# Kernel tuning notes

Hardware: AMD Instinct MI355X
Metric: run time of the kernel (lower is better)

## Reference

```python
import jax, jax.numpy as jnp
import numpy as np

N_NODES = 100000
N_EDGES = 1600000
IN_DIM = 128
HIDDEN = 128
EPS = 1e-5  # BatchNorm1d default eps


def gcn_conv(x, src, dst, W, b, n_nodes):
    """PyG GCNConv with default add_self_loops=True, edge_weight=None.
    out = D^{-1/2} (A + I) D^{-1/2} X W + b, deg computed from dst (col)."""
    xw = x @ W  # [N, out_dim] -- transform before propagate, as in PyG
    ones = jnp.ones((src.shape[0],), dtype=x.dtype)
    deg = jax.ops.segment_sum(ones, dst, num_segments=n_nodes) + 1.0  # +1 self-loop
    dis = jax.lax.rsqrt(deg)  # deg >= 1 always
    norm = dis[src] * dis[dst]  # [E]
    msgs = xw[src] * norm[:, None]  # [E, out_dim] gather (irregular access)
    agg = jax.ops.segment_sum(msgs, dst, num_segments=n_nodes)
    agg = agg + xw * (1.0 / deg)[:, None]  # self-loop contribution, norm = 1/deg_i
    return agg + b


def batch_norm(x, gamma, beta):
    # training-mode BatchNorm1d: biased batch statistics over the node dim
    m = jnp.mean(x, axis=0)
    v = jnp.mean(jnp.square(x - m), axis=0)
    return gamma * (x - m) * jax.lax.rsqrt(v + EPS) + beta


def setup_inputs() -> dict:
    key = jax.random.key(0)
    ks = jax.random.split(key, 6)
    x = jax.random.normal(ks[0], (N_NODES, IN_DIM), dtype=jnp.float32)
    edge_index = jax.random.randint(ks[1], (2, N_EDGES), 0, N_NODES, dtype=jnp.int64)
    # Glorot-ish scaled weights
    W1 = jax.random.normal(ks[2], (IN_DIM, HIDDEN), dtype=jnp.float32) / np.sqrt(IN_DIM)
    W2 = jax.random.normal(ks[3], (HIDDEN, HIDDEN // 2), dtype=jnp.float32) / np.sqrt(HIDDEN)
    Wf = jax.random.normal(ks[4], (HIDDEN // 2, 1), dtype=jnp.float32) / np.sqrt(HIDDEN // 2)
    return {
        "x": x,
        "edge_index": edge_index,
        "W1": W1, "b1": jnp.zeros((HIDDEN,), jnp.float32),
        "g1": jnp.ones((HIDDEN,), jnp.float32), "beta1": jnp.zeros((HIDDEN,), jnp.float32),
        "W2": W2, "b2": jnp.zeros((HIDDEN // 2,), jnp.float32),
        "g2": jnp.ones((HIDDEN // 2,), jnp.float32), "beta2": jnp.zeros((HIDDEN // 2,), jnp.float32),
        "Wf": Wf, "bf": jnp.zeros((1,), jnp.float32),
    }


def reference(x, edge_index, W1, b1, g1, beta1, W2, b2, g2, beta2, Wf, bf):
    src, dst = edge_index[0], edge_index[1]
    n = x.shape[0]
    h = jax.nn.relu(batch_norm(gcn_conv(x, src, dst, W1, b1, n), g1, beta1))
    # dropout is identity in eval / correctness-baseline mode
    h = jax.nn.relu(batch_norm(gcn_conv(h, src, dst, W2, b2, n), g2, beta2))
    return h @ Wf + bf  # [N, 1]
```

## Files before the change

kernel.cpp:

```cpp
#include <hip/hip_runtime.h>

#define NN 100000
#define NE 1600000
#define D1 128
#define D2 64
#define BN_EPS 1e-5f
#define SCAN_CHUNK 512
#define NB_SCAN ((NN + SCAN_CHUNK - 1) / SCAN_CHUNK)
#define NB_WT   ((128 * 128 + 64 * 128 + 255) / 256)
#define NB_FILL (NE / 512)
#define NB_G1   ((NN + 63) / 64)

typedef unsigned int uint32;
typedef unsigned short ushort;
typedef __attribute__((ext_vector_type(8))) short bf16x8;
typedef __attribute__((ext_vector_type(4))) float f32x4;

__device__ __forceinline__ ushort f2bf1(float f) {
    uint32 u = __float_as_uint(f);
    return (ushort)((u + 0x7FFFu + ((u >> 16) & 1u)) >> 16);
}
__device__ __forceinline__ uint32 f2bf_pair(float a, float b) {
    uint32 ua = __float_as_uint(a), ub = __float_as_uint(b);
    ua = (ua + 0x7FFFu + ((ua >> 16) & 1u)) >> 16;
    ub = (ub + 0x7FFFu + ((ub >> 16) & 1u)) >> 16;
    return ua | (ub << 16);
}
__device__ __forceinline__ float bf_lo(uint32 v) { return __uint_as_float(v << 16); }
__device__ __forceinline__ float bf_hi(uint32 v) { return __uint_as_float(v & 0xFFFF0000u); }

__global__ __launch_bounds__(256) void wtcnt_k(const float* __restrict__ W1,
                                               const float* __restrict__ W2,
                                               ushort* __restrict__ wt1,
                                               ushort* __restrict__ wt2,
                                               const int* __restrict__ dst,
                                               int* __restrict__ cnt) {
    if (blockIdx.x < NB_WT) {
        int i = blockIdx.x * 256 + threadIdx.x;
        if (i < 128 * 128) {
            int c = i >> 7, k = i & 127;
            wt1[i] = f2bf1(W1[k * 128 + c]);
        } else if (i < 128 * 128 + 64 * 128) {
            int o = i - 128 * 128;
            int c = o >> 7, k = o & 127;
            wt2[o] = f2bf1(W2[k * 64 + c]);
        }
        return;
    }
    int i = (blockIdx.x - NB_WT) * 256 + threadIdx.x;
    int2 dd = *(const int2*)&dst[2 * i];
    atomicAdd(&cnt[dd.x], 1);
    atomicAdd(&cnt[dd.y], 1);
}

__global__ __launch_bounds__(SCAN_CHUNK) void scan1_k(const int* __restrict__ cnt,
                                                      int* __restrict__ rowptr,
                                                      int* __restrict__ bsum,
                                                      float* __restrict__ dis) {
    __shared__ int sh[SCAN_CHUNK];
    int tid = threadIdx.x;
    int g = blockIdx.x * SCAN_CHUNK + tid;
    int v = (g < NN) ? cnt[g] : 0;
    if (g < NN) dis[g] = rsqrtf((float)v + 1.0f);
    sh[tid] = v;
    __syncthreads();
    for (int o = 1; o < SCAN_CHUNK; o <<= 1) {
        int t = (tid >= o) ? sh[tid - o] : 0;
        __syncthreads();
        sh[tid] += t;
        __syncthreads();
    }
    if (g < NN) rowptr[g] = sh[tid] - v;
    if (tid == SCAN_CHUNK - 1) bsum[blockIdx.x] = sh[tid];
}

__global__ __launch_bounds__(256) void scan23_k(int* __restrict__ rowptr,
                                                const int* __restrict__ bsum) {
    __shared__ int bs[256];
    int tid = threadIdx.x;
    bs[tid] = (tid < NB_SCAN) ? bsum[tid] : 0;
    __syncthreads();
    for (int o = 1; o < 256; o <<= 1) {
        int t = (tid >= o) ? bs[tid - o] : 0;
        __syncthreads();
        bs[tid] += t;
        __syncthreads();
    }
    int g = blockIdx.x * 256 + tid;
    if (g < NN) {
        int chunk = g >> 9;
        int add = (chunk == 0) ? 0 : bs[chunk - 1];
        rowptr[g] += add;
    }
    if (g == 0) rowptr[NN] = NE;
}

__global__ __launch_bounds__(256) void fillgemm_k(const int* __restrict__ src,
                                                  const int* __restrict__ dst,
                                                  const int* __restrict__ rowptr,
                                                  int* __restrict__ cur,
                                                  int* __restrict__ esrc,
                                                  const float* __restrict__ X,
                                                  const ushort* __restrict__ Wt,
                                                  ushort* __restrict__ Yb) {
    if (blockIdx.x < NB_FILL) {
        int i = blockIdx.x * 256 + threadIdx.x;
        int2 ss = *(const int2*)&src[2 * i];
        int2 dd = *(const int2*)&dst[2 * i];
        int p0 = rowptr[dd.x] + atomicAdd(&cur[dd.x], 1);
        esrc[p0] = ss.x;
        int p1 = rowptr[dd.y] + atomicAdd(&cur[dd.y], 1);
        esrc[p1] = ss.y;
        return;
    }
    const int bid = blockIdx.x - NB_FILL;
    const int lane = threadIdx.x & 63;
    const int wv = threadIdx.x >> 6;
    const int row0 = bid * 64 + wv * 16;
    const int m = lane & 15;
    const int kg = lane >> 4;
    const int rowA = min(row0 + m, NN - 1);
    f32x4 acc[8];
    #pragma unroll
    for (int t = 0; t < 8; ++t) acc[t] = (f32x4){0.f, 0.f, 0.f, 0.f};

    #pragma unroll
    for (int kc = 0; kc < 128; kc += 32) {
        const int k0 = kc + kg * 8;
        float4 xa = *(const float4*)(X + (size_t)rowA * 128 + k0);
        float4 xb = *(const float4*)(X + (size_t)rowA * 128 + k0 + 4);
        bf16x8 af;
        af[0] = (short)f2bf1(xa.x); af[1] = (short)f2bf1(xa.y);
        af[2] = (short)f2bf1(xa.z); af[3] = (short)f2bf1(xa.w);
        af[4] = (short)f2bf1(xb.x); af[5] = (short)f2bf1(xb.y);
        af[6] = (short)f2bf1(xb.z); af[7] = (short)f2bf1(xb.w);
        #pragma unroll
        for (int t = 0; t < 8; ++t) {
            bf16x8 bfr = *(const bf16x8*)(Wt + (size_t)(t * 16 + m) * 128 + k0);
            acc[t] = __builtin_amdgcn_mfma_f32_16x16x32_bf16(af, bfr, acc[t], 0, 0, 0);
        }
    }
    #pragma unroll
    for (int t = 0; t < 8; ++t)
        #pragma unroll
        for (int r = 0; r < 4; ++r) {
            int rr = row0 + kg * 4 + r;
            if (rr < NN) Yb[(size_t)rr * 128 + t * 16 + m] = f2bf1(acc[t][r]);
        }
}

__global__ __launch_bounds__(256) void mgemm2_k(const ushort* __restrict__ Xb,
                                                const ushort* __restrict__ Wt,
                                                const float* __restrict__ sums,
                                                const float* __restrict__ ssq,
                                                const float* __restrict__ g,
                                                const float* __restrict__ beta,
                                                ushort* __restrict__ Yb) {
    __shared__ float sc[128], shf[128];
    {
        int t = threadIdx.x;
        if (t < 128) {
            float m = sums[t] * (1.0f / NN);
            float var = ssq[t] * (1.0f / NN) - m * m;
            float s = g[t] * rsqrtf(var + BN_EPS);
            sc[t] = s;
            shf[t] = beta[t] - m * s;
        }
    }
    __syncthreads();
    const int lane = threadIdx.x & 63;
    const int wv = threadIdx.x >> 6;
    const int row0 = blockIdx.x * 64 + wv * 16;
    const int m = lane & 15;
    const int kg = lane >> 4;
    const int rowA = min(row0 + m, NN - 1);
    f32x4 acc[4];
    #pragma unroll
    for (int t = 0; t < 4; ++t) acc[t] = (f32x4){0.f, 0.f, 0.f, 0.f};

    #pragma unroll
    for (int kc = 0; kc < 128; kc += 32) {
        const int k0 = kc + kg * 8;
        uint4 raw = *(const uint4*)(Xb + (size_t)rowA * 128 + k0);
        float xs[8];
        xs[0] = bf_lo(raw.x); xs[1] = bf_hi(raw.x);
        xs[2] = bf_lo(raw.y); xs[3] = bf_hi(raw.y);
        xs[4] = bf_lo(raw.z); xs[5] = bf_hi(raw.z);
        xs[6] = bf_lo(raw.w); xs[7] = bf_hi(raw.w);
        float4 sa = *(const float4*)&sc[k0];
        float4 sb = *(const float4*)&sc[k0 + 4];
        float4 ha = *(const float4*)&shf[k0];
        float4 hb = *(const float4*)&shf[k0 + 4];
        xs[0] = fmaxf(fmaf(xs[0], sa.x, ha.x), 0.f);
        xs[1] = fmaxf(fmaf(xs[1], sa.y, ha.y), 0.f);
        xs[2] = fmaxf(fmaf(xs[2], sa.z, ha.z), 0.f);
        xs[3] = fmaxf(fmaf(xs[3], sa.w, ha.w), 0.f);
        xs[4] = fmaxf(fmaf(xs[4], sb.x, hb.x), 0.f);
        xs[5] = fmaxf(fmaf(xs[5], sb.y, hb.y), 0.f);
        xs[6] = fmaxf(fmaf(xs[6], sb.z, hb.z), 0.f);
        xs[7] = fmaxf(fmaf(xs[7], sb.w, hb.w), 0.f);
        bf16x8 af;
        #pragma unroll
        for (int i = 0; i < 8; ++i) af[i] = (short)f2bf1(xs[i]);
        #pragma unroll
        for (int t = 0; t < 4; ++t) {
            bf16x8 bfr = *(const bf16x8*)(Wt + (size_t)(t * 16 + m) * 128 + k0);
            acc[t] = __builtin_amdgcn_mfma_f32_16x16x32_bf16(af, bfr, acc[t], 0, 0, 0);
        }
    }
    #pragma unroll
    for (int t = 0; t < 4; ++t)
        #pragma unroll
        for (int r = 0; r < 4; ++r) {
            int rr = row0 + kg * 4 + r;
            if (rr < NN) Yb[(size_t)rr * 64 + t * 16 + m] = f2bf1(acc[t][r]);
        }
}

__global__ __launch_bounds__(256) void agg128_k(const int* __restrict__ rowptr,
                                                const int* __restrict__ esrc,
                                                const float* __restrict__ dis,
                                                const uint32* __restrict__ xwb,
                                                const float* __restrict__ b,
                                                uint32* __restrict__ agg1b,
                                                float* __restrict__ sums,
                                                float* __restrict__ ssq) {
    const int lane = threadIdx.x & 63;
    const int wid = (blockIdx.x * 256 + threadIdx.x) >> 6;
    const int nwaves = gridDim.x * 4;
    float s0 = 0.f, s1 = 0.f, q0 = 0.f, q1 = 0.f;
    const float bc0 = b[lane * 2], bc1 = b[lane * 2 + 1];

    for (int n = wid; n < NN; n += nwaves) {
        const int beg = rowptr[n], end = rowptr[n + 1];
        const float dn = dis[n];
        float ax = 0.f, ay = 0.f;
        int e = beg;
        for (; e + 8 <= end; e += 8) {
            int idx[8]; uint32 vv[8]; float w[8];
            #pragma unroll
            for (int j = 0; j < 8; ++j) idx[j] = esrc[e + j];
            #pragma unroll
            for (int j = 0; j < 8; ++j)
                vv[j] = xwb[(size_t)idx[j] * 64 + lane];
            #pragma unroll
            for (int j = 0; j < 8; ++j) w[j] = dis[idx[j]] * dn;
            #pragma unroll
            for (int j = 0; j < 8; ++j) {
                ax = fmaf(bf_lo(vv[j]), w[j], ax);
                ay = fmaf(bf_hi(vv[j]), w[j], ay);
            }
        }
        for (; e < end; ++e) {
            int s = esrc[e];
            float w = dis[s] * dn;
            uint32 v = xwb[(size_t)s * 64 + lane];
            ax = fmaf(bf_lo(v), w, ax);
            ay = fmaf(bf_hi(v), w, ay);
        }
        float sl = dn * dn;
        uint32 xv = xwb[(size_t)n * 64 + lane];
        ax = fmaf(bf_lo(xv), sl, ax) + bc0;
        ay = fmaf(bf_hi(xv), sl, ay) + bc1;
        agg1b[(size_t)n * 64 + lane] = f2bf_pair(ax, ay);
        s0 += ax; q0 = fmaf(ax, ax, q0);
        s1 += ay; q1 = fmaf(ay, ay, q1);
    }

    __shared__ float ls[256];
    ls[threadIdx.x] = 0.f;
    __syncthreads();
    atomicAdd(&ls[lane * 2], s0);
    atomicAdd(&ls[lane * 2 + 1], s1);
    atomicAdd(&ls[128 + lane * 2], q0);
    atomicAdd(&ls[128 + lane * 2 + 1], q1);
    __syncthreads();
    if (threadIdx.x < 128) atomicAdd(&sums[threadIdx.x], ls[threadIdx.x]);
    else atomicAdd(&ssq[threadIdx.x - 128], ls[threadIdx.x]);
}

__global__ __launch_bounds__(256) void agg64_k(const int* __restrict__ rowptr,
                                               const int* __restrict__ esrc,
                                               const float* __restrict__ dis,
                                               const uint32* __restrict__ xwb,
                                               const float* __restrict__ b,
                                               uint32* __restrict__ agg2b,
                                               float* __restrict__ sums,
                                               float* __restrict__ ssq) {
    const int lane = threadIdx.x & 63;
    const int half = lane >> 5;
    const int sl = lane & 31;
    const int wid = (blockIdx.x * 256 + threadIdx.x) >> 6;
    const int nwaves = gridDim.x * 4;
    float s0 = 0.f, s1 = 0.f, q0 = 0.f, q1 = 0.f;
    const float bc0 = b[sl * 2], bc1 = b[sl * 2 + 1];

    for (int n = wid; n < NN; n += nwaves) {
        const int beg = rowptr[n], end = rowptr[n + 1];
        const float dn = dis[n];
        float ax = 0.f, ay = 0.f;
        int e = beg;
        for (; e + 16 <= end; e += 16) {
            int idx[8]; uint32 vv[8]; float w[8];
            #pragma unroll
            for (int j = 0; j < 8; ++j) idx[j] = esrc[e + 2 * j + half];
            #pragma unroll
            for (int j = 0; j < 8; ++j)
                vv[j] = xwb[(size_t)idx[j] * 32 + sl];
            #pragma unroll
            for (int j = 0; j < 8; ++j) w[j] = dis[idx[j]] * dn;
            #pragma unroll
            for (int j = 0; j < 8; ++j) {
                ax = fmaf(bf_lo(vv[j]), w[j], ax);
                ay = fmaf(bf_hi(vv[j]), w[j], ay);
            }
        }
        for (; e + 2 <= end; e += 2) {
            int s = esrc[e + half];
            float w = dis[s] * dn;
            uint32 v = xwb[(size_t)s * 32 + sl];
            ax = fmaf(bf_lo(v), w, ax);
            ay = fmaf(bf_hi(v), w, ay);
        }
        if (e < end && half == 0) {
            int s = esrc[e];
            float w = dis[s] * dn;
            uint32 v = xwb[(size_t)s * 32 + sl];
            ax = fmaf(bf_lo(v), w, ax);
            ay = fmaf(bf_hi(v), w, ay);
        }
        ax += __shfl_down(ax, 32);
        ay += __shfl_down(ay, 32);
        if (half == 0) {
            float slf = dn * dn;
            uint32 xv = xwb[(size_t)n * 32 + sl];
            ax = fmaf(bf_lo(xv), slf, ax) + bc0;
            ay = fmaf(bf_hi(xv), slf, ay) + bc1;
            agg2b[(size_t)n * 32 + sl] = f2bf_pair(ax, ay);
            s0 += ax; q0 = fmaf(ax, ax, q0);
            s1 += ay; q1 = fmaf(ay, ay, q1);
        }
    }

    __shared__ float ls[128];
    if (threadIdx.x < 128) ls[threadIdx.x] = 0.f;
    __syncthreads();
    if (half == 0) {
        atomicAdd(&ls[sl * 2], s0);
        atomicAdd(&ls[sl * 2 + 1], s1);
        atomicAdd(&ls[64 + sl * 2], q0);
        atomicAdd(&ls[64 + sl * 2 + 1], q1);
    }
    __syncthreads();
    if (threadIdx.x < 64) atomicAdd(&sums[threadIdx.x], ls[threadIdx.x]);
    else if (threadIdx.x < 128) atomicAdd(&ssq[threadIdx.x - 64], ls[threadIdx.x]);
}

__global__ __launch_bounds__(256) void final_k(const uint32* __restrict__ h2b,
                                               const float* __restrict__ sums,
                                               const float* __restrict__ ssq,
                                               const float* __restrict__ g,
                                               const float* __restrict__ beta,
                                               const float* __restrict__ Wf,
                                               const float* __restrict__ bf,
                                               float* __restrict__ out) {
    __shared__ float sc[64], shf[64];
    {
        int t = threadIdx.x;
        if (t < 64) {
            float m = sums[t] * (1.0f / NN);
            float var = ssq[t] * (1.0f / NN) - m * m;
            float s = g[t] * rsqrtf(var + BN_EPS);
            sc[t] = s;
            shf[t] = beta[t] - m * s;
        }
    }
    __syncthreads();
    const int lane = threadIdx.x & 63;
    const int half = lane >> 5;
    const int sl = lane & 31;
    const int node = ((blockIdx.x * 256 + threadIdx.x) >> 6) * 2 + half;
    if (node >= NN) return;
    uint32 p = h2b[(size_t)node * 32 + sl];
    float2 wf = *(const float2*)&Wf[sl * 2];
    float v = fmaxf(fmaf(bf_lo(p), sc[sl * 2], shf[sl * 2]), 0.f) * wf.x;
    v = fmaf(fmaxf(fmaf(bf_hi(p), sc[sl * 2 + 1], shf[sl * 2 + 1]), 0.f), wf.y, v);
    #pragma unroll
    for (int o = 16; o > 0; o >>= 1) v += __shfl_down(v, o, 32);
    if (sl == 0) out[node] = v + bf[0];
}

extern "C" void kernel_launch(void* const* d_in, const int* in_sizes, int n_in,
                              void* d_out, int out_size, void* d_ws, size_t ws_size,
                              hipStream_t stream) {
    const float* x   = (const float*)d_in[0];
    const int*   ei  = (const int*)d_in[1];
    const int*   src = ei;
    const int*   dst = ei + NE;
    const float* W1  = (const float*)d_in[2];
    const float* b1  = (const float*)d_in[3];
    const float* g1  = (const float*)d_in[4];
    const float* be1 = (const float*)d_in[5];
    const float* W2  = (const float*)d_in[6];
    const float* b2  = (const float*)d_in[7];
    const float* g2  = (const float*)d_in[8];
    const float* be2 = (const float*)d_in[9];
    const float* Wf  = (const float*)d_in[10];
    const float* bf  = (const float*)d_in[11];
    float* out = (float*)d_out;

    uint32* xwb   = (uint32*)d_ws;
    uint32* agg1b = xwb + (size_t)NN * 64;
    uint32* agg2b = agg1b + (size_t)NN * 64;
    float*  dis   = (float*)(agg2b + (size_t)NN * 32);
    ushort* wt1   = (ushort*)(dis + NN);
    ushort* wt2   = wt1 + 128 * 128;
    int*    rowptr = (int*)(wt2 + 64 * 128);
    int*    bsum   = rowptr + NN + 1;
    int*    esrc   = bsum + 256;
    int*    cnt    = esrc + NE;
    int*    cur    = cnt + NN;
    float*  sums1  = (float*)(cur + NN);
    float*  ssq1   = sums1 + D1;
    float*  sums2  = ssq1 + D1;
    float*  ssq2   = sums2 + D2;

    hipMemsetAsync(cnt, 0, sizeof(int) * (2 * NN + 2 * D1 + 2 * D2), stream);

    wtcnt_k<<<NB_WT + NE / 512, 256, 0, stream>>>(W1, W2, wt1, wt2, dst, cnt);
    scan1_k<<<NB_SCAN, SCAN_CHUNK, 0, stream>>>(cnt, rowptr, bsum, dis);
    scan23_k<<<(NN + 255) / 256, 256, 0, stream>>>(rowptr, bsum);

    fillgemm_k<<<NB_FILL + NB_G1, 256, 0, stream>>>(src, dst, rowptr, cur, esrc,
                                                    x, wt1, (ushort*)xwb);

    agg128_k<<<2048, 256, 0, stream>>>(rowptr, esrc, dis, xwb, b1, agg1b, sums1, ssq1);

    mgemm2_k<<<(NN + 63) / 64, 256, 0, stream>>>((const ushort*)agg1b, wt2, sums1, ssq1,
                                                 g1, be1, (ushort*)xwb);
    agg64_k<<<2048, 256, 0, stream>>>(rowptr, esrc, dis, xwb, b2, agg2b, sums2, ssq2);

    final_k<<<(NN / 2 + 3) / 4, 256, 0, stream>>>(agg2b, sums2, ssq2, g2, be2, Wf, bf, out);
}
```

Measured before the change: 521.6 us.

## Pack per-edge normalization weight with source index in CSR edge array

During CSR fill, each edge now stores a 64-bit word that packs the source index with the precomputed weight dis[src]*dis[dst]. Both aggregation kernels read this word, so they no longer do a random gather from dis per edge. The aggregation loops also drop their scalar tail loops and instead run a clamped, masked 8-wide batch. In exchange the edge array doubles in size to 64 bits per edge, and the fill kernel does extra random reads of dis.

```diff
diff --git a/kernel.cpp b/kernel.cpp
--- a/kernel.cpp
+++ b/kernel.cpp
@@ -12,6 +12,7 @@
 #define NB_G1   ((NN + 63) / 64)
 
 typedef unsigned int uint32;
+typedef unsigned long long u64;
 typedef unsigned short ushort;
 typedef __attribute__((ext_vector_type(8))) short bf16x8;
 typedef __attribute__((ext_vector_type(4))) float f32x4;
@@ -98,8 +99,9 @@
 __global__ __launch_bounds__(256) void fillgemm_k(const int* __restrict__ src,
                                                   const int* __restrict__ dst,
                                                   const int* __restrict__ rowptr,
+                                                  const float* __restrict__ dis,
                                                   int* __restrict__ cur,
-                                                  int* __restrict__ esrc,
+                                                  u64* __restrict__ edges,
                                                   const float* __restrict__ X,
                                                   const ushort* __restrict__ Wt,
                                                   ushort* __restrict__ Yb) {
@@ -107,10 +109,12 @@
         int i = blockIdx.x * 256 + threadIdx.x;
         int2 ss = *(const int2*)&src[2 * i];
         int2 dd = *(const int2*)&dst[2 * i];
+        u64 pk0 = ((u64)__float_as_uint(dis[ss.x] * dis[dd.x]) << 32) | (uint32)ss.x;
         int p0 = rowptr[dd.x] + atomicAdd(&cur[dd.x], 1);
-        esrc[p0] = ss.x;
+        edges[p0] = pk0;
+        u64 pk1 = ((u64)__float_as_uint(dis[ss.y] * dis[dd.y]) << 32) | (uint32)ss.y;
         int p1 = rowptr[dd.y] + atomicAdd(&cur[dd.y], 1);
-        esrc[p1] = ss.y;
+        edges[p1] = pk1;
         return;
     }
     const int bid = blockIdx.x - NB_FILL;
@@ -218,7 +222,7 @@
 }
 
 __global__ __launch_bounds__(256) void agg128_k(const int* __restrict__ rowptr,
-                                                const int* __restrict__ esrc,
+                                                const u64* __restrict__ edges,
                                                 const float* __restrict__ dis,
                                                 const uint32* __restrict__ xwb,
                                                 const float* __restrict__ b,
@@ -235,28 +239,21 @@
         const int beg = rowptr[n], end = rowptr[n + 1];
         const float dn = dis[n];
         float ax = 0.f, ay = 0.f;
-        int e = beg;
-        for (; e + 8 <= end; e += 8) {
-            int idx[8]; uint32 vv[8]; float w[8];
-            #pragma unroll
-            for (int j = 0; j < 8; ++j) idx[j] = esrc[e + j];
+        for (int e = beg; e < end; e += 8) {
+            u64 ed[8]; uint32 vv[8]; float w[8];
+            #pragma unroll
+            for (int j = 0; j < 8; ++j) ed[j] = edges[min(e + j, end - 1)];
             #pragma unroll
             for (int j = 0; j < 8; ++j)
-                vv[j] = xwb[(size_t)idx[j] * 64 + lane];
-            #pragma unroll
-            for (int j = 0; j < 8; ++j) w[j] = dis[idx[j]] * dn;
+                vv[j] = xwb[(size_t)(uint32)ed[j] * 64 + lane];
+            #pragma unroll
+            for (int j = 0; j < 8; ++j)
+                w[j] = (e + j < end) ? __uint_as_float((uint32)(ed[j] >> 32)) : 0.f;
             #pragma unroll
             for (int j = 0; j < 8; ++j) {
                 ax = fmaf(bf_lo(vv[j]), w[j], ax);
                 ay = fmaf(bf_hi(vv[j]), w[j], ay);
             }
-        }
-        for (; e < end; ++e) {
-            int s = esrc[e];
-            float w = dis[s] * dn;
-            uint32 v = xwb[(size_t)s * 64 + lane];
-            ax = fmaf(bf_lo(v), w, ax);
-            ay = fmaf(bf_hi(v), w, ay);
         }
         float sl = dn * dn;
         uint32 xv = xwb[(size_t)n * 64 + lane];
@@ -280,7 +277,7 @@
 }
 
 __global__ __launch_bounds__(256) void agg64_k(const int* __restrict__ rowptr,
-                                               const int* __restrict__ esrc,
+                                               const u64* __restrict__ edges,
                                                const float* __restrict__ dis,
                                                const uint32* __restrict__ xwb,
                                                const float* __restrict__ b,
@@ -299,35 +296,21 @@
         const int beg = rowptr[n], end = rowptr[n + 1];
         const float dn = dis[n];
         float ax = 0.f, ay = 0.f;
-        int e = beg;
-        for (; e + 16 <= end; e += 16) {
-            int idx[8]; uint32 vv[8]; float w[8];
-            #pragma unroll
-            for (int j = 0; j < 8; ++j) idx[j] = esrc[e + 2 * j + half];
+        for (int e = beg; e < end; e += 16) {
+            u64 ed[8]; uint32 vv[8]; float w[8];
+            #pragma unroll
+            for (int j = 0; j < 8; ++j) ed[j] = edges[min(e + 2 * j + half, end - 1)];
             #pragma unroll
             for (int j = 0; j < 8; ++j)
-                vv[j] = xwb[(size_t)idx[j] * 32 + sl];
-            #pragma unroll
-            for (int j = 0; j < 8; ++j) w[j] = dis[idx[j]] * dn;
+                vv[j] = xwb[(size_t)(uint32)ed[j] * 32 + sl];
+            #pragma unroll
+            for (int j = 0; j < 8; ++j)
+                w[j] = (e + 2 * j + half < end) ? __uint_as_float((uint32)(ed[j] >> 32)) : 0.f;
             #pragma unroll
             for (int j = 0; j < 8; ++j) {
                 ax = fmaf(bf_lo(vv[j]), w[j], ax);
                 ay = fmaf(bf_hi(vv[j]), w[j], ay);
             }
-        }
-        for (; e + 2 <= end; e += 2) {
-            int s = esrc[e + half];
-            float w = dis[s] * dn;
-            uint32 v = xwb[(size_t)s * 32 + sl];
-            ax = fmaf(bf_lo(v), w, ax);
-            ay = fmaf(bf_hi(v), w, ay);
-        }
-        if (e < end && half == 0) {
-            int s = esrc[e];
-            float w = dis[s] * dn;
-            uint32 v = xwb[(size_t)s * 32 + sl];
-            ax = fmaf(bf_lo(v), w, ax);
-            ay = fmaf(bf_hi(v), w, ay);
         }
         ax += __shfl_down(ax, 32);
         ay += __shfl_down(ay, 32);
@@ -417,8 +400,8 @@
     ushort* wt2   = wt1 + 128 * 128;
     int*    rowptr = (int*)(wt2 + 64 * 128);
     int*    bsum   = rowptr + NN + 1;
-    int*    esrc   = bsum + 256;
-    int*    cnt    = esrc + NE;
+    u64*    edges  = (u64*)(((size_t)(bsum + 256) + 7) & ~(size_t)7);
+    int*    cnt    = (int*)(edges + NE);
     int*    cur    = cnt + NN;
     float*  sums1  = (float*)(cur + NN);
     float*  ssq1   = sums1 + D1;
@@ -431,14 +414,14 @@
     scan1_k<<<NB_SCAN, SCAN_CHUNK, 0, stream>>>(cnt, rowptr, bsum, dis);
     scan23_k<<<(NN + 255) / 256, 256, 0, stream>>>(rowptr, bsum);
 
-    fillgemm_k<<<NB_FILL + NB_G1, 256, 0, stream>>>(src, dst, rowptr, cur, esrc,
+    fillgemm_k<<<NB_FILL + NB_G1, 256, 0, stream>>>(src, dst, rowptr, dis, cur, edges,
                                                     x, wt1, (ushort*)xwb);
 
-    agg128_k<<<2048, 256, 0, stream>>>(rowptr, esrc, dis, xwb, b1, agg1b, sums1, ssq1);
+    agg128_k<<<2048, 256, 0, stream>>>(rowptr, edges, dis, xwb, b1, agg1b, sums1, ssq1);
 
     mgemm2_k<<<(NN + 63) / 64, 256, 0, stream>>>((const ushort*)agg1b, wt2, sums1, ssq1,
                                                  g1, be1, (ushort*)xwb);
-    agg64_k<<<2048, 256, 0, stream>>>(rowptr, esrc, dis, xwb, b2, agg2b, sums2, ssq2);
+    agg64_k<<<2048, 256, 0, stream>>>(rowptr, edges, dis, xwb, b2, agg2b, sums2, ssq2);
 
     final_k<<<(NN / 2 + 3) / 4, 256, 0, stream>>>(agg2b, sums2, ssq2, g2, be2, Wf, bf, out);
 }
```

After: 447.4 us. -14.2%, faster.
